# Optimization experiments

Hardware: AMD Instinct MI355X
Metric: run time of the kernel (lower is better)

## Reference

```python
import jax, jax.numpy as jnp
import numpy as np

EPS = 1e-5

def layernorm(x, g, b):
    xf = x.astype(jnp.float32)
    mu = jnp.mean(xf, axis=-1, keepdims=True)
    var = jnp.mean(jnp.square(xf - mu), axis=-1, keepdims=True)
    return ((xf - mu) * jax.lax.rsqrt(var + EPS) * g + b).astype(x.dtype)

def setup_inputs() -> dict:
    key = jax.random.key(0)
    ks = jax.random.split(key, 8)
    B, L, D_NODE, D_PAIR = 2, 512, 256, 128
    single = jax.random.normal(ks[0], (B, L, D_NODE), dtype=jnp.float32)
    pair = jax.random.normal(ks[1], (B, L, L, D_PAIR), dtype=jnp.float32)
    s = 1.0 / np.sqrt(D_NODE)
    Wa = jax.random.normal(ks[2], (D_PAIR, D_NODE), dtype=jnp.float32) * s
    ba = jnp.zeros((D_PAIR,), jnp.float32)
    Wb = jax.random.normal(ks[3], (D_PAIR, D_NODE), dtype=jnp.float32) * s
    bb = jnp.zeros((D_PAIR,), jnp.float32)
    # out layer is init='final' (zeros) in the original; use small random weights
    # so the reference output is non-trivial (same math).
    Wo = jax.random.normal(ks[4], (D_PAIR, D_PAIR), dtype=jnp.float32) * (1.0 / np.sqrt(D_PAIR))
    bo = jnp.zeros((D_PAIR,), jnp.float32)
    norm_g = jnp.ones((D_NODE,), jnp.float32)
    norm_b = jnp.zeros((D_NODE,), jnp.float32)
    pnorm_g = jnp.ones((D_PAIR,), jnp.float32)
    pnorm_b = jnp.zeros((D_PAIR,), jnp.float32)
    return dict(single=single, pair=pair, norm_g=norm_g, norm_b=norm_b,
                Wa=Wa, ba=ba, Wb=Wb, bb=bb, Wo=Wo, bo=bo,
                pnorm_g=pnorm_g, pnorm_b=pnorm_b)

def reference(single, pair, norm_g, norm_b, Wa, ba, Wb, bb, Wo, bo, pnorm_g, pnorm_b):
    x = layernorm(single, norm_g, norm_b)          # (B, L, D_NODE)
    a = x @ Wa.T + ba                               # (B, L, D_PAIR)
    b = x @ Wb.T + bb                               # (B, L, D_PAIR)
    outer = jnp.einsum('bid,bjd->bijd', a, b)       # (B, L, L, D_PAIR)
    upd = outer @ Wo.T + bo                         # (B, L, L, D_PAIR)
    return layernorm(pair + upd, pnorm_g, pnorm_b)
```

## Files before the change

kernel.cpp:

```cpp
#include <hip/hip_runtime.h>

#define BB   2
#define LL   512
#define DN   256
#define DP   128
#define TJ   64
#define LDSW 136

using bf16x8 = __attribute__((ext_vector_type(8))) short;
using f32x4  = __attribute__((ext_vector_type(4))) float;

__device__ inline unsigned short f2bf(float f) {
    unsigned int u = __float_as_uint(f);
    u += 0x7FFFu + ((u >> 16) & 1u);
    return (unsigned short)(u >> 16);
}

__global__ __launch_bounds__(256) void pu_ln_ab(
    const float* __restrict__ single, const float* __restrict__ norm_g,
    const float* __restrict__ norm_b, const float* __restrict__ Wa,
    const float* __restrict__ ba, const float* __restrict__ Wb,
    const float* __restrict__ bbias, float* __restrict__ abuf,
    unsigned short* __restrict__ bbuf)
{
    __shared__ __attribute__((aligned(16))) float xs[DN];
    __shared__ float red[8];
    const int row = blockIdx.x;
    const int tid = threadIdx.x;

    float v = single[row * DN + tid];
    float s1 = v, s2 = v * v;
    #pragma unroll
    for (int m = 32; m; m >>= 1) {
        s1 += __shfl_xor(s1, m);
        s2 += __shfl_xor(s2, m);
    }
    const int w = tid >> 6;
    if ((tid & 63) == 0) { red[w] = s1; red[4 + w] = s2; }
    __syncthreads();
    s1 = red[0] + red[1] + red[2] + red[3];
    s2 = red[4] + red[5] + red[6] + red[7];
    const float mu  = s1 * (1.0f / DN);
    const float var = s2 * (1.0f / DN) - mu * mu;
    const float rs  = rsqrtf(var + 1e-5f);
    xs[tid] = (v - mu) * rs * norm_g[tid] + norm_b[tid];
    __syncthreads();

    const int half = tid >> 7, p = tid & 127;
    const float4* W4 = (const float4*)((half ? Wb : Wa) + p * DN);
    const float4* x4 = (const float4*)xs;
    float acc = 0.f;
    #pragma unroll 8
    for (int d = 0; d < DN / 4; d++) {
        float4 wv = W4[d], xv = x4[d];
        acc += wv.x * xv.x + wv.y * xv.y + wv.z * xv.z + wv.w * xv.w;
    }
    acc += (half ? bbias[p] : ba[p]);
    if (half == 0) abuf[row * DP + p] = acc;
    else           bbuf[row * DP + p] = f2bf(acc);
}

__global__ __launch_bounds__(256) void pu_outer_ln(
    const float* __restrict__ pr, const float* __restrict__ Wo,
    const float* __restrict__ bo, const float* __restrict__ png,
    const float* __restrict__ pnb, const float* __restrict__ abuf,
    const unsigned short* __restrict__ bbuf, float* __restrict__ out)
{
    __shared__ __attribute__((aligned(16))) unsigned short sW[DP * LDSW];
    __shared__ __attribute__((aligned(16))) unsigned short sB[TJ * LDSW];

    const int jt  = blockIdx.x;
    const int i   = blockIdx.y;
    const int bz  = blockIdx.z;
    const int tid = threadIdx.x;
    const int j0  = jt * TJ;

    const int lane = tid & 63;
    const int w    = tid >> 6;
    const int m    = lane & 15;
    const int q    = lane >> 4;

    const size_t obase = (((size_t)bz * LL + i) * LL + (j0 + w * 16)) * DP;
    float pv[4][8];
    #pragma unroll
    for (int r = 0; r < 4; r++) {
        const size_t rowoff = obase + (size_t)(q * 4 + r) * DP + m;
        #pragma unroll
        for (int t = 0; t < 8; t++) pv[r][t] = pr[rowoff + t * 16];
    }

    float bo_r[8], g_r[8], pb_r[8];
    #pragma unroll
    for (int t = 0; t < 8; t++) {
        bo_r[t] = bo[t * 16 + m];
        g_r[t]  = png[t * 16 + m];
        pb_r[t] = pnb[t * 16 + m];
    }

    const float* arow = abuf + ((size_t)bz * LL + i) * DP;
    #pragma unroll
    for (int e = 0; e < 8; e++) {
        const int v  = tid + e * 256;
        const int pw = v >> 4;
        const int d0 = (v & 15) * 8;
        const float4* w4 = (const float4*)(Wo + pw * DP + d0);
        const float4* a4 = (const float4*)(arow + d0);
        float4 wa = w4[0], wb = w4[1], aa = a4[0], ab = a4[1];
        uint4 pk;
        pk.x = (unsigned)f2bf(wa.x * aa.x) | ((unsigned)f2bf(wa.y * aa.y) << 16);
        pk.y = (unsigned)f2bf(wa.z * aa.z) | ((unsigned)f2bf(wa.w * aa.w) << 16);
        pk.z = (unsigned)f2bf(wb.x * ab.x) | ((unsigned)f2bf(wb.y * ab.y) << 16);
        pk.w = (unsigned)f2bf(wb.z * ab.z) | ((unsigned)f2bf(wb.w * ab.w) << 16);
        *(uint4*)&sW[pw * LDSW + d0] = pk;
    }

    const uint4* bsrc = (const uint4*)(bbuf + ((size_t)bz * LL + j0) * DP);
    #pragma unroll
    for (int e = 0; e < 4; e++) {
        const int v  = tid + e * 256;
        const int jr = v >> 4;
        const int d0 = (v & 15) * 8;
        *(uint4*)&sB[jr * LDSW + d0] = bsrc[v];
    }
    __syncthreads();

    f32x4 acc[8];
    #pragma unroll
    for (int t = 0; t < 8; t++) { f32x4 z = {0.f, 0.f, 0.f, 0.f}; acc[t] = z; }

    const unsigned short* Abase = sB + (w * 16 + m) * LDSW + q * 8;
    const unsigned short* Bbase = sW + m * LDSW + q * 8;
    #pragma unroll
    for (int s = 0; s < 4; s++) {
        bf16x8 af = *(const bf16x8*)(Abase + s * 32);
        #pragma unroll
        for (int t = 0; t < 8; t++) {
            bf16x8 bf = *(const bf16x8*)(Bbase + t * 16 * LDSW + s * 32);
            acc[t] = __builtin_amdgcn_mfma_f32_16x16x32_bf16(af, bf, acc[t], 0, 0, 0);
        }
    }

    #pragma unroll
    for (int r = 0; r < 4; r++) {
        const size_t rowoff = obase + (size_t)(q * 4 + r) * DP + m;
        float v[8], s1 = 0.f, s2 = 0.f;
        #pragma unroll
        for (int t = 0; t < 8; t++) {
            v[t] = pv[r][t] + acc[t][r] + bo_r[t];
            s1 += v[t];
            s2 += v[t] * v[t];
        }
        s1 += __shfl_xor(s1, 1); s2 += __shfl_xor(s2, 1);
        s1 += __shfl_xor(s1, 2); s2 += __shfl_xor(s2, 2);
        s1 += __shfl_xor(s1, 4); s2 += __shfl_xor(s2, 4);
        s1 += __shfl_xor(s1, 8); s2 += __shfl_xor(s2, 8);
        const float mu  = s1 * (1.0f / DP);
        const float var = s2 * (1.0f / DP) - mu * mu;
        const float rs  = rsqrtf(var + 1e-5f);
        #pragma unroll
        for (int t = 0; t < 8; t++)
            out[rowoff + t * 16] = (v[t] - mu) * rs * g_r[t] + pb_r[t];
    }
}

extern "C" void kernel_launch(void* const* d_in, const int* in_sizes, int n_in,
                              void* d_out, int out_size, void* d_ws, size_t ws_size,
                              hipStream_t stream) {
    const float* single = (const float*)d_in[0];
    const float* pair   = (const float*)d_in[1];
    const float* norm_g = (const float*)d_in[2];
    const float* norm_b = (const float*)d_in[3];
    const float* Wa     = (const float*)d_in[4];
    const float* ba     = (const float*)d_in[5];
    const float* Wb     = (const float*)d_in[6];
    const float* bb     = (const float*)d_in[7];
    const float* Wo     = (const float*)d_in[8];
    const float* bo     = (const float*)d_in[9];
    const float* png    = (const float*)d_in[10];
    const float* pnb    = (const float*)d_in[11];
    float* out = (float*)d_out;

    float* abuf = (float*)d_ws;
    unsigned short* bbuf =
        (unsigned short*)((char*)d_ws + (size_t)BB * LL * DP * sizeof(float));

    pu_ln_ab<<<dim3(BB * LL), dim3(256), 0, stream>>>(
        single, norm_g, norm_b, Wa, ba, Wb, bb, abuf, bbuf);

    pu_outer_ln<<<dim3(LL / TJ, LL, BB), dim3(256), 0, stream>>>(
        pair, Wo, bo, png, pnb, abuf, bbuf, out);
}
```

Before: 527.7 us.

## Transpose MFMA operands so pair rows load and store as float4

The MFMA operands are swapped so that each lane's accumulator holds four contiguous feature columns of a single pair row. Pair loads and output stores become 16-byte vector accesses with nontemporal hints, replacing strided scalar accesses. The b-tile now goes straight from global memory into registers, which removes its LDS staging buffer, and the LayerNorm reduction becomes two cross-lane shuffles. Launch bounds now request 4 blocks per CU, which may constrain register allocation.

```diff
diff --git a/kernel.cpp b/kernel.cpp
--- a/kernel.cpp
+++ b/kernel.cpp
@@ -60,42 +60,38 @@
     else           bbuf[row * DP + p] = f2bf(acc);
 }
 
-__global__ __launch_bounds__(256) void pu_outer_ln(
+__global__ __launch_bounds__(256, 4) void pu_outer_ln(
     const float* __restrict__ pr, const float* __restrict__ Wo,
     const float* __restrict__ bo, const float* __restrict__ png,
     const float* __restrict__ pnb, const float* __restrict__ abuf,
     const unsigned short* __restrict__ bbuf, float* __restrict__ out)
 {
     __shared__ __attribute__((aligned(16))) unsigned short sW[DP * LDSW];
-    __shared__ __attribute__((aligned(16))) unsigned short sB[TJ * LDSW];
 
     const int jt  = blockIdx.x;
     const int i   = blockIdx.y;
     const int bz  = blockIdx.z;
     const int tid = threadIdx.x;
-    const int j0  = jt * TJ;
 
     const int lane = tid & 63;
     const int w    = tid >> 6;
     const int m    = lane & 15;
     const int q    = lane >> 4;
 
-    const size_t obase = (((size_t)bz * LL + i) * LL + (j0 + w * 16)) * DP;
-    float pv[4][8];
+    const int jrow = jt * TJ + w * 16 + m;
+    const size_t rowbase = (((size_t)bz * LL + i) * LL + jrow) * DP;
+    const int p0 = q * 4;
+
+    f32x4 pv[8];
     #pragma unroll
-    for (int r = 0; r < 4; r++) {
-        const size_t rowoff = obase + (size_t)(q * 4 + r) * DP + m;
-        #pragma unroll
-        for (int t = 0; t < 8; t++) pv[r][t] = pr[rowoff + t * 16];
-    }
+    for (int t = 0; t < 8; t++)
+        pv[t] = __builtin_nontemporal_load((const f32x4*)(pr + rowbase + t * 16 + p0));
 
-    float bo_r[8], g_r[8], pb_r[8];
+    const unsigned short* brow = bbuf + ((size_t)bz * LL + jrow) * DP + q * 8;
+    bf16x8 bfrag[4];
     #pragma unroll
-    for (int t = 0; t < 8; t++) {
-        bo_r[t] = bo[t * 16 + m];
-        g_r[t]  = png[t * 16 + m];
-        pb_r[t] = pnb[t * 16 + m];
-    }
+    for (int s = 0; s < 4; s++)
+        bfrag[s] = *(const bf16x8*)(brow + s * 32);
 
     const float* arow = abuf + ((size_t)bz * LL + i) * DP;
     #pragma unroll
@@ -113,53 +109,48 @@
         pk.w = (unsigned)f2bf(wb.z * ab.z) | ((unsigned)f2bf(wb.w * ab.w) << 16);
         *(uint4*)&sW[pw * LDSW + d0] = pk;
     }
-
-    const uint4* bsrc = (const uint4*)(bbuf + ((size_t)bz * LL + j0) * DP);
-    #pragma unroll
-    for (int e = 0; e < 4; e++) {
-        const int v  = tid + e * 256;
-        const int jr = v >> 4;
-        const int d0 = (v & 15) * 8;
-        *(uint4*)&sB[jr * LDSW + d0] = bsrc[v];
-    }
     __syncthreads();
 
     f32x4 acc[8];
     #pragma unroll
     for (int t = 0; t < 8; t++) { f32x4 z = {0.f, 0.f, 0.f, 0.f}; acc[t] = z; }
 
-    const unsigned short* Abase = sB + (w * 16 + m) * LDSW + q * 8;
-    const unsigned short* Bbase = sW + m * LDSW + q * 8;
+    const unsigned short* Ab = sW + m * LDSW + q * 8;
     #pragma unroll
     for (int s = 0; s < 4; s++) {
-        bf16x8 af = *(const bf16x8*)(Abase + s * 32);
         #pragma unroll
         for (int t = 0; t < 8; t++) {
-            bf16x8 bf = *(const bf16x8*)(Bbase + t * 16 * LDSW + s * 32);
-            acc[t] = __builtin_amdgcn_mfma_f32_16x16x32_bf16(af, bf, acc[t], 0, 0, 0);
+            bf16x8 af = *(const bf16x8*)(Ab + t * 16 * LDSW + s * 32);
+            acc[t] = __builtin_amdgcn_mfma_f32_16x16x32_bf16(af, bfrag[s], acc[t], 0, 0, 0);
         }
     }
 
+    float s1 = 0.f, s2 = 0.f;
     #pragma unroll
-    for (int r = 0; r < 4; r++) {
-        const size_t rowoff = obase + (size_t)(q * 4 + r) * DP + m;
-        float v[8], s1 = 0.f, s2 = 0.f;
-        #pragma unroll
-        for (int t = 0; t < 8; t++) {
-            v[t] = pv[r][t] + acc[t][r] + bo_r[t];
-            s1 += v[t];
-            s2 += v[t] * v[t];
-        }
-        s1 += __shfl_xor(s1, 1); s2 += __shfl_xor(s2, 1);
-        s1 += __shfl_xor(s1, 2); s2 += __shfl_xor(s2, 2);
-        s1 += __shfl_xor(s1, 4); s2 += __shfl_xor(s2, 4);
-        s1 += __shfl_xor(s1, 8); s2 += __shfl_xor(s2, 8);
-        const float mu  = s1 * (1.0f / DP);
-        const float var = s2 * (1.0f / DP) - mu * mu;
-        const float rs  = rsqrtf(var + 1e-5f);
-        #pragma unroll
-        for (int t = 0; t < 8; t++)
-            out[rowoff + t * 16] = (v[t] - mu) * rs * g_r[t] + pb_r[t];
+    for (int t = 0; t < 8; t++) {
+        float4 b4 = *(const float4*)(bo + t * 16 + p0);
+        f32x4 v = pv[t] + acc[t];
+        v.x += b4.x; v.y += b4.y; v.z += b4.z; v.w += b4.w;
+        pv[t] = v;
+        s1 += v.x + v.y + v.z + v.w;
+        s2 += v.x * v.x + v.y * v.y + v.z * v.z + v.w * v.w;
+    }
+    s1 += __shfl_xor(s1, 16); s2 += __shfl_xor(s2, 16);
+    s1 += __shfl_xor(s1, 32); s2 += __shfl_xor(s2, 32);
+    const float mu  = s1 * (1.0f / DP);
+    const float var = s2 * (1.0f / DP) - mu * mu;
+    const float rs  = rsqrtf(var + 1e-5f);
+
+    #pragma unroll
+    for (int t = 0; t < 8; t++) {
+        float4 g4  = *(const float4*)(png + t * 16 + p0);
+        float4 pb4 = *(const float4*)(pnb + t * 16 + p0);
+        f32x4 o;
+        o.x = (pv[t].x - mu) * rs * g4.x + pb4.x;
+        o.y = (pv[t].y - mu) * rs * g4.y + pb4.y;
+        o.z = (pv[t].z - mu) * rs * g4.z + pb4.z;
+        o.w = (pv[t].w - mu) * rs * g4.w + pb4.w;
+        __builtin_nontemporal_store(o, (f32x4*)(out + rowbase + t * 16 + p0));
     }
 }
 
```

Measured after the change: 553.0 us. 4.8% more time.
